# Kernel optimization log

Measured on AMD Instinct MI355X. Metric: run time of the kernel, lower is better.

## Reference

```python
import jax, jax.numpy as jnp
import numpy as np

B, T, C, H = 2, 2048, 1024, 16
HD = C // H
EPS = 1e-5


def _gelu_tanh(x):
    # 0.5*x*(1+tanh(sqrt(2/pi)*(x+0.044715*x^3)))
    c = jnp.sqrt(jnp.asarray(2.0 / np.pi, dtype=x.dtype))
    return 0.5 * x * (1.0 + jnp.tanh(c * (x + 0.044715 * x * x * x)))


def _layernorm(x, g, b):
    mu = jnp.mean(x, axis=-1, keepdims=True)
    var = jnp.mean(jnp.square(x - mu), axis=-1, keepdims=True)
    return (x - mu) * jax.lax.rsqrt(var + EPS) * g + b


def setup_inputs() -> dict:
    key = jax.random.key(0)
    ks = jax.random.split(key, 8)
    s = lambda fan_in: 1.0 / np.sqrt(fan_in)
    return {
        "x": jax.random.normal(ks[0], (B, T, C), jnp.float32),
        "ln1_g": jnp.ones((C,), jnp.float32),
        "ln1_b": jnp.zeros((C,), jnp.float32),
        "W_attn": jax.random.normal(ks[1], (C, 3 * C), jnp.float32) * s(C),
        "b_attn": jnp.zeros((3 * C,), jnp.float32),
        "W_proj": jax.random.normal(ks[2], (C, C), jnp.float32) * s(C),
        "b_proj": jnp.zeros((C,), jnp.float32),
        "ln2_g": jnp.ones((C,), jnp.float32),
        "ln2_b": jnp.zeros((C,), jnp.float32),
        "W_fc": jax.random.normal(ks[3], (C, 4 * C), jnp.float32) * s(C),
        "b_fc": jnp.zeros((4 * C,), jnp.float32),
        "W_fc2": jax.random.normal(ks[4], (4 * C, C), jnp.float32) * s(4 * C),
        "b_fc2": jnp.zeros((C,), jnp.float32),
    }


def reference(x, ln1_g, ln1_b, W_attn, b_attn, W_proj, b_proj,
              ln2_g, ln2_b, W_fc, b_fc, W_fc2, b_fc2):
    # --- attention branch (pre-LN) ---
    h = _layernorm(x, ln1_g, ln1_b)
    qkv = h @ W_attn + b_attn                      # [B,T,3C]
    q, k, v = jnp.split(qkv, 3, axis=2)
    q = q.reshape(B, T, H, HD).transpose(0, 2, 1, 3)  # [B,H,T,HD]
    k = k.reshape(B, T, H, HD).transpose(0, 2, 1, 3)
    v = v.reshape(B, T, H, HD).transpose(0, 2, 1, 3)
    att = jnp.einsum('bhqd,bhkd->bhqk', q, k) / jnp.sqrt(jnp.asarray(HD, x.dtype))
    causal = jnp.tril(jnp.ones((T, T), bool))
    att = jnp.where(causal, att, jnp.asarray(-jnp.inf, att.dtype))
    att = jax.nn.softmax(att, axis=-1)
    y = jnp.einsum('bhqk,bhkd->bhqd', att, v)      # [B,H,T,HD]
    y = y.transpose(0, 2, 1, 3).reshape(B, T, C)
    x = x + (y @ W_proj + b_proj)
    # --- MLP branch (pre-LN) ---
    h = _layernorm(x, ln2_g, ln2_b)
    h = _gelu_tanh(h @ W_fc + b_fc)
    x = x + (h @ W_fc2 + b_fc2)
    return x
```

## Files before the change

### kernel.cpp

```cpp
#include <hip/hip_runtime.h>
#include <hip/hip_bf16.h>
#include <cstdint>
#include <cstddef>

#define B_  2
#define T_  2048
#define C_  1024
#define H_  16
#define HD_ 64
#define M_TOT 4096

typedef __bf16 bf16x8 __attribute__((ext_vector_type(8)));
typedef float  f32x4  __attribute__((ext_vector_type(4)));
typedef unsigned short u16;

__device__ __forceinline__ u16 f2bf(float f) {
  __hip_bfloat16 h = __float2bfloat16(f);
  return __builtin_bit_cast(u16, h);
}

__device__ __forceinline__ void async_cp16(const u16* g, u16* l) {
  __builtin_amdgcn_global_load_lds(
      (const __attribute__((address_space(1))) void*)g,
      (__attribute__((address_space(3))) void*)l, 16, 0, 0);
}

__device__ __forceinline__ float gelu_f(float x) {
  const float z = 0.7978845608028654f * (x + 0.044715f * x * x * x);
  return x / (1.0f + __expf(-2.0f * z));
}

__global__ __launch_bounds__(256) void ln_bf16_kernel(
    const float* __restrict__ x, const float* __restrict__ g,
    const float* __restrict__ b, u16* __restrict__ out) {
  const int row = blockIdx.x;
  const int tid = threadIdx.x;
  const float4 v = reinterpret_cast<const float4*>(x)[row * 256 + tid];
  float s  = v.x + v.y + v.z + v.w;
  float sq = v.x * v.x + v.y * v.y + v.z * v.z + v.w * v.w;
#pragma unroll
  for (int off = 32; off > 0; off >>= 1) {
    s  += __shfl_xor(s, off);
    sq += __shfl_xor(sq, off);
  }
  __shared__ float red[8];
  const int wave = tid >> 6;
  if ((tid & 63) == 0) { red[wave] = s; red[4 + wave] = sq; }
  __syncthreads();
  s  = red[0] + red[1] + red[2] + red[3];
  sq = red[4] + red[5] + red[6] + red[7];
  const float mu   = s * (1.0f / 1024.0f);
  const float rstd = rsqrtf(sq * (1.0f / 1024.0f) - mu * mu + 1e-5f);
  const float4 gv = reinterpret_cast<const float4*>(g)[tid];
  const float4 bv = reinterpret_cast<const float4*>(b)[tid];
  ushort4 o;
  o.x = f2bf((v.x - mu) * rstd * gv.x + bv.x);
  o.y = f2bf((v.y - mu) * rstd * gv.y + bv.y);
  o.z = f2bf((v.z - mu) * rstd * gv.z + bv.z);
  o.w = f2bf((v.w - mu) * rstd * gv.w + bv.w);
  reinterpret_cast<ushort4*>(out)[row * 256 + tid] = o;
}

__global__ __launch_bounds__(256) void transpose_bf16_kernel(
    const float* __restrict__ W, u16* __restrict__ Wt, int K, int N) {
  __shared__ float tile[32][33];
  const int n0 = blockIdx.x * 32, k0 = blockIdx.y * 32;
  const int tx = threadIdx.x & 31;
  const int ty = threadIdx.x >> 5;
#pragma unroll
  for (int i = 0; i < 4; ++i)
    tile[ty + 8 * i][tx] = W[(k0 + ty + 8 * i) * (size_t)N + n0 + tx];
  __syncthreads();
#pragma unroll
  for (int i = 0; i < 4; ++i)
    Wt[(n0 + ty + 8 * i) * (size_t)K + k0 + tx] = f2bf(tile[tx][ty + 8 * i]);
}

template <int MODE, int BM>
__global__ __launch_bounds__(256, 2) void gemm_kernel(
    const u16* __restrict__ A, const u16* __restrict__ Bt,
    const float* __restrict__ bias, const float* __restrict__ resid,
    float* __restrict__ outf, u16* __restrict__ outb,
    u16* __restrict__ qo, u16* __restrict__ ko, u16* __restrict__ vto,
    int M, int N, int K) {
  constexpr int MT = BM / 32;
  __shared__ __align__(16) u16 As[BM * 32];
  __shared__ __align__(16) u16 Bs[128 * 32];
  const int tid  = threadIdx.x;
  const int wave = tid >> 6, lane = tid & 63;
  const int col  = lane & 15, quad = lane >> 4;
  const int wm   = wave >> 1, wn = wave & 1;
  const int bn = blockIdx.x, bm = blockIdx.y;

  const int ar = bm * BM + wave * (BM / 4) + (lane >> 2);
  const int br = bn * 128 + wave * 32 + (lane >> 2);
  const int kc = (lane & 3) * 8;
  const u16* ap = A  + (size_t)ar * K + kc;
  const u16* bp = Bt + (size_t)br * K + kc;
  u16* as_dst = As + wave * (BM / 4) * 32;
  u16* bs_dst = Bs + wave * 1024;

  f32x4 acc[MT][4] = {};

  for (int k0 = 0; k0 < K; k0 += 32) {
    __syncthreads();
    async_cp16(ap + k0, as_dst);
    if constexpr (BM == 128) async_cp16(ap + 16 * K + k0, as_dst + 512);
    async_cp16(bp + k0,          bs_dst);
    async_cp16(bp + 16 * K + k0, bs_dst + 512);
    __syncthreads();
    bf16x8 af[MT], bf[4];
#pragma unroll
    for (int mt = 0; mt < MT; ++mt)
      af[mt] = *reinterpret_cast<const bf16x8*>(&As[(wm * (BM / 2) + mt * 16 + col) * 32 + quad * 8]);
#pragma unroll
    for (int nt = 0; nt < 4; ++nt)
      bf[nt] = *reinterpret_cast<const bf16x8*>(&Bs[(wn * 64 + nt * 16 + col) * 32 + quad * 8]);
#pragma unroll
    for (int mt = 0; mt < MT; ++mt)
#pragma unroll
      for (int nt = 0; nt < 4; ++nt)
        acc[mt][nt] = __builtin_amdgcn_mfma_f32_16x16x32_bf16(af[mt], bf[nt], acc[mt][nt], 0, 0, 0);
  }

#pragma unroll
  for (int mt = 0; mt < MT; ++mt) {
#pragma unroll
    for (int r = 0; r < 4; ++r) {
      const int grow = bm * BM + wm * (BM / 2) + mt * 16 + quad * 4 + r;
#pragma unroll
      for (int nt = 0; nt < 4; ++nt) {
        const int gcol = bn * 128 + wn * 64 + nt * 16 + col;
        const float val = acc[mt][nt][r] + bias[gcol];
        if constexpr (MODE == 0) {
          outb[(size_t)grow * N + gcol] = f2bf(gelu_f(val));
        } else if constexpr (MODE == 1) {
          outf[(size_t)grow * N + gcol] = resid[(size_t)grow * N + gcol] + val;
        } else {
          const int which = gcol >> 10, c = gcol & 1023;
          const int hh = c >> 6, dd = c & 63;
          const int bb = grow >> 11, tt = grow & 2047;
          if (which == 0)
            qo[((bb * H_ + hh) * (size_t)T_ + tt) * HD_ + dd] = f2bf(val * 0.125f);
          else if (which == 1)
            ko[((bb * H_ + hh) * (size_t)T_ + tt) * HD_ + dd] = f2bf(val);
          else
            vto[((bb * H_ + hh) * (size_t)HD_ + dd) * T_ + tt] = f2bf(val);
        }
      }
    }
  }
}

#define PSTR 68
__global__ __launch_bounds__(256, 4) void attn_kernel(
    const u16* __restrict__ q, const u16* __restrict__ k,
    const u16* __restrict__ vt, u16* __restrict__ y) {
  const int bh  = blockIdx.x;
  const int qt  = (T_ / 64 - 1) - blockIdx.y;
  const int tid = threadIdx.x;
  const int wave = tid >> 6, lane = tid & 63;
  const int col = lane & 15, quad = lane >> 4;
  const int b = bh >> 4, h = bh & 15;
  const int r0w = qt * 64 + wave * 16;

  __shared__ __align__(16) u16 Klds[64 * PSTR];
  __shared__ __align__(16) u16 Vtlds[64 * PSTR];
  __shared__ __align__(16) u16 Plds[4 * 16 * PSTR];

  bf16x8 aq[2];
#pragma unroll
  for (int j = 0; j < 2; ++j)
    aq[j] = *reinterpret_cast<const bf16x8*>(
        &q[((size_t)bh * T_ + r0w + col) * HD_ + j * 32 + quad * 8]);

  bf16x8 ones;
#pragma unroll
  for (int jj = 0; jj < 8; ++jj) ones[jj] = (__bf16)1.0f;

  f32x4 o[4] = {};
  f32x4 l_acc = {};

  const int srow = tid >> 3, spart = tid & 7;
  u16* pw = Plds + wave * 16 * PSTR;
  const u16* kbase  = k  + (size_t)bh * T_ * HD_ + srow * HD_ + spart * 8;
  const u16* vtbase = vt + (size_t)bh * HD_ * T_ + srow * T_ + spart * 8;

  const int kb_last = qt * 64;

  uint4 kv0, kv1, kv2, kv3;
  kv0 = *reinterpret_cast<const uint4*>(kbase);
  kv1 = *reinterpret_cast<const uint4*>(kbase + 32 * HD_);
  kv2 = *reinterpret_cast<const uint4*>(vtbase);
  kv3 = *reinterpret_cast<const uint4*>(vtbase + 32 * T_);

  for (int kb = 0; kb <= kb_last; kb += 64) {
    *reinterpret_cast<uint4*>(&Klds[srow * PSTR + spart * 8])        = kv0;
    *reinterpret_cast<uint4*>(&Klds[(srow + 32) * PSTR + spart * 8]) = kv1;
    *reinterpret_cast<uint4*>(&Vtlds[srow * PSTR + spart * 8])        = kv2;
    *reinterpret_cast<uint4*>(&Vtlds[(srow + 32) * PSTR + spart * 8]) = kv3;
    __syncthreads();

    if (kb < kb_last) {
      const int nk = kb + 64;
      kv0 = *reinterpret_cast<const uint4*>(kbase + (size_t)nk * HD_);
      kv1 = *reinterpret_cast<const uint4*>(kbase + (size_t)(nk + 32) * HD_ - 32 * HD_ + 32 * HD_);
      kv1 = *reinterpret_cast<const uint4*>(kbase + (size_t)nk * HD_ + 32 * HD_);
      kv2 = *reinterpret_cast<const uint4*>(vtbase + nk);
      kv3 = *reinterpret_cast<const uint4*>(vtbase + 32 * T_ + nk);
    }

    f32x4 s[4];
#pragma unroll
    for (int n = 0; n < 4; ++n) {
      const bf16x8 bk0 = *reinterpret_cast<const bf16x8*>(&Klds[(n * 16 + col) * PSTR + quad * 8]);
      const bf16x8 bk1 = *reinterpret_cast<const bf16x8*>(&Klds[(n * 16 + col) * PSTR + 32 + quad * 8]);
      f32x4 z = {};
      z = __builtin_amdgcn_mfma_f32_16x16x32_bf16(aq[0], bk0, z, 0, 0, 0);
      s[n] = __builtin_amdgcn_mfma_f32_16x16x32_bf16(aq[1], bk1, z, 0, 0, 0);
    }

    const bool domask = (kb == kb_last);
#pragma unroll
    for (int n = 0; n < 4; ++n) {
#pragma unroll
      for (int r = 0; r < 4; ++r) {
        float sv = s[n][r];
        if (domask) {
          const int key = kb + n * 16 + col;
          const int row = r0w + quad * 4 + r;
          sv = (key <= row) ? sv : -1e30f;
        }
        pw[(quad * 4 + r) * PSTR + n * 16 + col] = f2bf(__expf(sv));
      }
    }
    __builtin_amdgcn_s_waitcnt(0xC07F);

    const bf16x8 ap0 = *reinterpret_cast<const bf16x8*>(&pw[col * PSTR + quad * 8]);
    const bf16x8 ap1 = *reinterpret_cast<const bf16x8*>(&pw[col * PSTR + 32 + quad * 8]);
    l_acc = __builtin_amdgcn_mfma_f32_16x16x32_bf16(ap0, ones, l_acc, 0, 0, 0);
    l_acc = __builtin_amdgcn_mfma_f32_16x16x32_bf16(ap1, ones, l_acc, 0, 0, 0);
#pragma unroll
    for (int n = 0; n < 4; ++n) {
      const bf16x8 bv0 = *reinterpret_cast<const bf16x8*>(&Vtlds[(n * 16 + col) * PSTR + quad * 8]);
      const bf16x8 bv1 = *reinterpret_cast<const bf16x8*>(&Vtlds[(n * 16 + col) * PSTR + 32 + quad * 8]);
      o[n] = __builtin_amdgcn_mfma_f32_16x16x32_bf16(ap0, bv0, o[n], 0, 0, 0);
      o[n] = __builtin_amdgcn_mfma_f32_16x16x32_bf16(ap1, bv1, o[n], 0, 0, 0);
    }
    __syncthreads();
  }

#pragma unroll
  for (int r = 0; r < 4; ++r) {
    const int qrow = r0w + quad * 4 + r;
    const float inv = 1.0f / l_acc[r];
#pragma unroll
    for (int n = 0; n < 4; ++n)
      y[((size_t)b * T_ + qrow) * C_ + h * HD_ + n * 16 + col] = f2bf(o[n][r] * inv);
  }
}

extern "C" void kernel_launch(void* const* d_in, const int* in_sizes, int n_in,
                              void* d_out, int out_size, void* d_ws, size_t ws_size,
                              hipStream_t stream) {
  const float* x      = (const float*)d_in[0];
  const float* ln1_g  = (const float*)d_in[1];
  const float* ln1_b  = (const float*)d_in[2];
  const float* W_attn = (const float*)d_in[3];
  const float* b_attn = (const float*)d_in[4];
  const float* W_proj = (const float*)d_in[5];
  const float* b_proj = (const float*)d_in[6];
  const float* ln2_g  = (const float*)d_in[7];
  const float* ln2_b  = (const float*)d_in[8];
  const float* W_fc   = (const float*)d_in[9];
  const float* b_fc   = (const float*)d_in[10];
  const float* W_fc2  = (const float*)d_in[11];
  const float* b_fc2  = (const float*)d_in[12];
  float* out = (float*)d_out;

  char* p = (char*)d_ws;
  auto alloc = [&](size_t bytes) {
    char* r = p;
    p += (bytes + 255) & ~(size_t)255;
    return r;
  };
  u16*   h1      = (u16*)alloc((size_t)M_TOT * C_ * 2);
  u16*   wt_attn = (u16*)alloc((size_t)3 * C_ * C_ * 2);
  u16*   wt_proj = (u16*)alloc((size_t)C_ * C_ * 2);
  u16*   wt_fc   = (u16*)alloc((size_t)4 * C_ * C_ * 2);
  u16*   wt_fc2  = (u16*)alloc((size_t)C_ * 4 * C_ * 2);
  u16*   qbuf    = (u16*)alloc((size_t)M_TOT * C_ * 2);
  u16*   kbuf    = (u16*)alloc((size_t)M_TOT * C_ * 2);
  u16*   vtbuf   = (u16*)alloc((size_t)M_TOT * C_ * 2);
  u16*   ybuf    = (u16*)alloc((size_t)M_TOT * C_ * 2);
  float* x2      = (float*)alloc((size_t)M_TOT * C_ * 4);
  u16*   h2      = (u16*)alloc((size_t)M_TOT * C_ * 2);
  u16*   act     = (u16*)alloc((size_t)M_TOT * 4 * C_ * 2);

  transpose_bf16_kernel<<<dim3(96, 32),  256, 0, stream>>>(W_attn, wt_attn, 1024, 3072);
  transpose_bf16_kernel<<<dim3(32, 32),  256, 0, stream>>>(W_proj, wt_proj, 1024, 1024);
  transpose_bf16_kernel<<<dim3(128, 32), 256, 0, stream>>>(W_fc,   wt_fc,   1024, 4096);
  transpose_bf16_kernel<<<dim3(32, 128), 256, 0, stream>>>(W_fc2,  wt_fc2,  4096, 1024);

  ln_bf16_kernel<<<M_TOT, 256, 0, stream>>>(x, ln1_g, ln1_b, h1);

  gemm_kernel<3, 128><<<dim3(24, 32), 256, 0, stream>>>(h1, wt_attn, b_attn, nullptr,
                                                        nullptr, nullptr, qbuf, kbuf, vtbuf,
                                                        4096, 3072, 1024);
  attn_kernel<<<dim3(32, 32), 256, 0, stream>>>(qbuf, kbuf, vtbuf, ybuf);

  gemm_kernel<1, 64><<<dim3(8, 64), 256, 0, stream>>>(ybuf, wt_proj, b_proj, x,
                                                      x2, nullptr, nullptr, nullptr, nullptr,
                                                      4096, 1024, 1024);
  ln_bf16_kernel<<<M_TOT, 256, 0, stream>>>(x2, ln2_g, ln2_b, h2);

  gemm_kernel<0, 128><<<dim3(32, 32), 256, 0, stream>>>(h2, wt_fc, b_fc, nullptr,
                                                        nullptr, act, nullptr, nullptr, nullptr,
                                                        4096, 4096, 1024);
  gemm_kernel<1, 64><<<dim3(8, 64), 256, 0, stream>>>(act, wt_fc2, b_fc2, x2,
                                                      out, nullptr, nullptr, nullptr, nullptr,
                                                      4096, 1024, 4096);
}
```

Measured before the change: 369.9 us.

## Deepen GEMM K-tile to 64, swizzle LDS, remap blocks across XCDs

The GEMM kernel now stages 64-wide K slices per iteration instead of 32, which halves the number of barrier pairs per tile. It applies an XOR swizzle to the LDS column index to avoid bank conflicts on the MFMA operand reads. It also remaps the flat block index so that each XCD gets a contiguous group of M-tiles, improving L2 reuse of A rows. The cost is doubled LDS per block, which may reduce occupancy, and the remapping depends on the grid sizes matching logPer.

```diff
diff --git a/kernel.cpp b/kernel.cpp
--- a/kernel.cpp
+++ b/kernel.cpp
@@ -82,45 +82,60 @@
     const float* __restrict__ bias, const float* __restrict__ resid,
     float* __restrict__ outf, u16* __restrict__ outb,
     u16* __restrict__ qo, u16* __restrict__ ko, u16* __restrict__ vto,
-    int M, int N, int K) {
+    int M, int N, int K, int logPer) {
   constexpr int MT = BM / 32;
-  __shared__ __align__(16) u16 As[BM * 32];
-  __shared__ __align__(16) u16 Bs[128 * 32];
+  constexpr int AI = BM / 32;
+  __shared__ __align__(16) u16 As[BM * 64];
+  __shared__ __align__(16) u16 Bs[128 * 64];
   const int tid  = threadIdx.x;
   const int wave = tid >> 6, lane = tid & 63;
   const int col  = lane & 15, quad = lane >> 4;
   const int wm   = wave >> 1, wn = wave & 1;
-  const int bn = blockIdx.x, bm = blockIdx.y;
-
-  const int ar = bm * BM + wave * (BM / 4) + (lane >> 2);
-  const int br = bn * 128 + wave * 32 + (lane >> 2);
-  const int kc = (lane & 3) * 8;
-  const u16* ap = A  + (size_t)ar * K + kc;
-  const u16* bp = Bt + (size_t)br * K + kc;
-  u16* as_dst = As + wave * (BM / 4) * 32;
-  u16* bs_dst = Bs + wave * 1024;
+
+  const int flat = blockIdx.y * gridDim.x + blockIdx.x;
+  const int xcd = flat & 7, sl = flat >> 3;
+  const int per = 1 << logPer;
+  const int bm = (xcd << logPer) + (sl & (per - 1));
+  const int bn = sl >> logPer;
+
+  const int srow = lane >> 3, sc8 = lane & 7;
+  const int kcs = (sc8 ^ srow) * 8;
+  const u16* ap = A  + (size_t)(bm * BM + wave * (BM / 4) + srow) * K + kcs;
+  const u16* bp = Bt + (size_t)(bn * 128 + wave * 32 + srow) * K + kcs;
+  u16* as_dst = As + wave * (BM / 4) * 64;
+  u16* bs_dst = Bs + wave * 2048;
 
   f32x4 acc[MT][4] = {};
 
-  for (int k0 = 0; k0 < K; k0 += 32) {
+  for (int k0 = 0; k0 < K; k0 += 64) {
     __syncthreads();
-    async_cp16(ap + k0, as_dst);
-    if constexpr (BM == 128) async_cp16(ap + 16 * K + k0, as_dst + 512);
-    async_cp16(bp + k0,          bs_dst);
-    async_cp16(bp + 16 * K + k0, bs_dst + 512);
+#pragma unroll
+    for (int i = 0; i < AI; ++i)
+      async_cp16(ap + k0 + i * 8 * (size_t)K, as_dst + i * 512);
+#pragma unroll
+    for (int i = 0; i < 4; ++i)
+      async_cp16(bp + k0 + i * 8 * (size_t)K, bs_dst + i * 512);
     __syncthreads();
-    bf16x8 af[MT], bf[4];
-#pragma unroll
-    for (int mt = 0; mt < MT; ++mt)
-      af[mt] = *reinterpret_cast<const bf16x8*>(&As[(wm * (BM / 2) + mt * 16 + col) * 32 + quad * 8]);
-#pragma unroll
-    for (int nt = 0; nt < 4; ++nt)
-      bf[nt] = *reinterpret_cast<const bf16x8*>(&Bs[(wn * 64 + nt * 16 + col) * 32 + quad * 8]);
-#pragma unroll
-    for (int mt = 0; mt < MT; ++mt)
-#pragma unroll
-      for (int nt = 0; nt < 4; ++nt)
-        acc[mt][nt] = __builtin_amdgcn_mfma_f32_16x16x32_bf16(af[mt], bf[nt], acc[mt][nt], 0, 0, 0);
+#pragma unroll
+    for (int kh = 0; kh < 2; ++kh) {
+      const int ks = kh * 4;
+      bf16x8 af[MT], bf[4];
+#pragma unroll
+      for (int mt = 0; mt < MT; ++mt) {
+        const int row = wm * (BM / 2) + mt * 16 + col;
+        af[mt] = *reinterpret_cast<const bf16x8*>(&As[row * 64 + ((ks + quad) ^ (col & 7)) * 8]);
+      }
+#pragma unroll
+      for (int nt = 0; nt < 4; ++nt) {
+        const int row = wn * 64 + nt * 16 + col;
+        bf[nt] = *reinterpret_cast<const bf16x8*>(&Bs[row * 64 + ((ks + quad) ^ (col & 7)) * 8]);
+      }
+#pragma unroll
+      for (int mt = 0; mt < MT; ++mt)
+#pragma unroll
+        for (int nt = 0; nt < 4; ++nt)
+          acc[mt][nt] = __builtin_amdgcn_mfma_f32_16x16x32_bf16(af[mt], bf[nt], acc[mt][nt], 0, 0, 0);
+    }
   }
 
 #pragma unroll
@@ -204,7 +219,6 @@
     if (kb < kb_last) {
       const int nk = kb + 64;
       kv0 = *reinterpret_cast<const uint4*>(kbase + (size_t)nk * HD_);
-      kv1 = *reinterpret_cast<const uint4*>(kbase + (size_t)(nk + 32) * HD_ - 32 * HD_ + 32 * HD_);
       kv1 = *reinterpret_cast<const uint4*>(kbase + (size_t)nk * HD_ + 32 * HD_);
       kv2 = *reinterpret_cast<const uint4*>(vtbase + nk);
       kv3 = *reinterpret_cast<const uint4*>(vtbase + 32 * T_ + nk);
@@ -306,18 +320,18 @@
 
   gemm_kernel<3, 128><<<dim3(24, 32), 256, 0, stream>>>(h1, wt_attn, b_attn, nullptr,
                                                         nullptr, nullptr, qbuf, kbuf, vtbuf,
-                                                        4096, 3072, 1024);
+                                                        4096, 3072, 1024, 2);
   attn_kernel<<<dim3(32, 32), 256, 0, stream>>>(qbuf, kbuf, vtbuf, ybuf);
 
   gemm_kernel<1, 64><<<dim3(8, 64), 256, 0, stream>>>(ybuf, wt_proj, b_proj, x,
                                                       x2, nullptr, nullptr, nullptr, nullptr,
-                                                      4096, 1024, 1024);
+                                                      4096, 1024, 1024, 3);
   ln_bf16_kernel<<<M_TOT, 256, 0, stream>>>(x2, ln2_g, ln2_b, h2);
 
   gemm_kernel<0, 128><<<dim3(32, 32), 256, 0, stream>>>(h2, wt_fc, b_fc, nullptr,
                                                         nullptr, act, nullptr, nullptr, nullptr,
-                                                        4096, 4096, 1024);
+                                                        4096, 4096, 1024, 2);
   gemm_kernel<1, 64><<<dim3(8, 64), 256, 0, stream>>>(act, wt_fc2, b_fc2, x2,
                                                       out, nullptr, nullptr, nullptr, nullptr,
-                                                      4096, 1024, 4096);
-}
+                                                      4096, 1024, 4096, 3);
+}
```

Result: faster. 338.4 us (-8.5%).
